# Performance work log

Measured on AMD Instinct MI355X. Metric: run time of the kernel, lower is better.

## Reference

```python
import jax, jax.numpy as jnp
import numpy as np

WIN = 8
NUM_HEADS = 4
DIM = 128


def _relative_position_index(ws):
    coords = np.stack(np.meshgrid(np.arange(ws), np.arange(ws), indexing='ij'))  # (2, ws, ws)
    cf = coords.reshape(2, -1)                      # (2, ws*ws)
    rel = (cf[:, :, None] - cf[:, None, :]).transpose(1, 2, 0).astype(np.int64)  # (N, N, 2)
    rel[..., 0] += ws - 1
    rel[..., 1] += ws - 1
    rel[..., 0] *= 2 * ws - 1
    return rel.sum(-1)                              # (N, N) int64


def setup_inputs() -> dict:
    key = jax.random.key(0)
    ks = jax.random.split(key, 8)
    B_, N, C = 4096, WIN * WIN, DIM
    nW = 4096
    x = jax.random.normal(ks[0], (B_, N, C), dtype=jnp.float32)
    mask = jax.random.normal(ks[1], (nW, N, N), dtype=jnp.float32)
    wq = jax.random.normal(ks[2], (C, C), dtype=jnp.float32) * 0.02
    bq = jnp.zeros((C,), dtype=jnp.float32)
    wkv = jax.random.normal(ks[3], (2 * C, C), dtype=jnp.float32) * 0.02
    bkv = jnp.zeros((2 * C,), dtype=jnp.float32)
    bias_table = jax.random.normal(ks[4], ((2 * WIN - 1) * (2 * WIN - 1), NUM_HEADS), dtype=jnp.float32) * 0.02
    wproj = jax.random.normal(ks[5], (C, C), dtype=jnp.float32) * 0.02
    bproj = jnp.zeros((C,), dtype=jnp.float32)
    rel_index = jnp.asarray(_relative_position_index(WIN))
    return {"x": x, "wq": wq, "bq": bq, "wkv": wkv, "bkv": bkv,
            "bias_table": bias_table, "wproj": wproj, "bproj": bproj,
            "mask": mask, "rel_index": rel_index}


def reference(x, wq, bq, wkv, bkv, bias_table, wproj, bproj, mask, rel_index):
    B_, N, C = x.shape
    H = NUM_HEADS
    d = C // H
    scale = d ** -0.5
    # qkv projection (attn_kv=None path)
    q = (x @ wq.T + bq).reshape(B_, N, H, d).transpose(0, 2, 1, 3)      # (B_, H, N, d)
    kv = (x @ wkv.T + bkv).reshape(B_, N, 2, H, d)
    k = kv[:, :, 0].transpose(0, 2, 1, 3)                               # (B_, H, N, d)
    v = kv[:, :, 1].transpose(0, 2, 1, 3)
    attn = jnp.einsum('bhnd,bhmd->bhnm', q * scale, k)                  # (B_, H, N, N)
    # relative position bias gather: (N*N,) -> (N, N, H) -> (H, N, N)
    rpb = bias_table[rel_index.reshape(-1)].reshape(N, N, H).transpose(2, 0, 1)
    attn = attn + rpb[None]
    # shifted-window mask: attn viewed as (B_//nW, nW, H, N, N) + mask (nW, 1, N, N)
    nW = mask.shape[0]
    attn = (attn.reshape(B_ // nW, nW, H, N, N) + mask[None, :, None]).reshape(B_, H, N, N)
    attn = jax.nn.softmax(attn, axis=-1)
    out = jnp.einsum('bhnm,bhmd->bhnd', attn, v).transpose(0, 2, 1, 3).reshape(B_, N, C)
    return out @ wproj.T + bproj
```

## Files before the change

kernel.cpp:

```cpp
#include <hip/hip_runtime.h>


typedef __bf16 bf16x8 __attribute__((ext_vector_type(8)));
typedef __bf16 bf16x4 __attribute__((ext_vector_type(4)));
typedef float f32x4 __attribute__((ext_vector_type(4)));

#define LOG2E 1.4426950408889634f
#define QSCALE (0.17677669529663687f * 1.4426950408889634f)

__global__ __launch_bounds__(256)
void prep_kernel(const float* __restrict__ wq,
                 const float* __restrict__ wkv,
                 const float* __restrict__ wp,
                 const float* __restrict__ bt,
                 const int* __restrict__ ri,
                 char* __restrict__ ws) {
  int t = blockIdx.x * 256 + (int)threadIdx.x;
  if (t < 8192) {
    int s = t >> 11;
    int c = t & 2047;
    int lane = c & 63, kk = (c >> 6) & 3, ct = c >> 8;
    int li = lane & 15, q4 = lane >> 4;
    int col = ct * 16 + li;
    int ko = kk * 32 + q4 * 8;
    const float* src = (s == 0) ? (wq + col * 128 + ko)
                     : (s == 1) ? (wkv + col * 128 + ko)
                     : (s == 2) ? (wkv + (col + 128) * 128 + ko)
                                : (wp + col * 128 + ko);
    bf16x8 v;
#pragma unroll
    for (int i = 0; i < 8; ++i) v[i] = (__bf16)src[i];
    *(bf16x8*)(ws + s * 32768 + c * 16) = v;
  } else {
    int c = t - 8192;
    int lane = c & 63, tj = (c >> 6) & 3, ti = (c >> 8) & 3, h = (c >> 10) & 3;
    int li = lane & 15, q4 = lane >> 4;
    int m = tj * 16 + li;
    f32x4 r;
#pragma unroll
    for (int rr = 0; rr < 4; ++rr) {
      int n = ti * 16 + q4 * 4 + rr;
      r[rr] = LOG2E * bt[ri[n * 64 + m] * 4 + h];
    }
    *(f32x4*)(ws + 131072 + c * 16) = r;
  }
}

static __device__ __forceinline__ bf16x8 cvt8(const float* __restrict__ p) {
  bf16x8 r;
#pragma unroll
  for (int i = 0; i < 8; ++i) r[i] = (__bf16)p[i];
  return r;
}

static __device__ __forceinline__ int xaddr(int r, int c) {
  return (r << 8) + ((((c >> 3) ^ (r & 7)) << 4)) + ((c & 7) << 1);
}
static __device__ __forceinline__ int qaddr(int r, int c) {
  return (r << 6) + ((((c >> 3) ^ ((r >> 2) & 3)) << 4)) + ((c & 7) << 1);
}
static __device__ __forceinline__ int paddr(int r, int c) {
  return (r << 7) + ((((c >> 3) ^ (r & 7)) << 4)) + ((c & 7) << 1);
}
static __device__ __forceinline__ int vtaddr(int dd, int m) {
  return (dd << 7) + ((((m >> 3) ^ (dd & 7)) << 4)) + ((m & 7) << 1);
}

#define MFMA16(acc, afr, bfr) \
  acc = __builtin_amdgcn_mfma_f32_16x16x32_bf16(afr, bfr, acc, 0, 0, 0)

__global__ __launch_bounds__(256, 3)
void winattn_kernel(const float* __restrict__ xg,
                    const float* __restrict__ bq,
                    const float* __restrict__ bkv,
                    const float* __restrict__ bp,
                    const float* __restrict__ mask,
                    const char* __restrict__ ws,
                    float* __restrict__ out) {
  __shared__ char smem[49152];
  const int b = blockIdx.x;
  const int tid = (int)threadIdx.x;
  const int h = tid >> 6;
  const int lane = tid & 63;
  const int q4 = lane >> 4;
  const int li = lane & 15;
  const int Wb = 16384 + h * 8192;
  const int Qb = Wb, Kb = Wb + 4096, Pb = Wb;
  const int Vb = h * 4096;
  const bf16x8* __restrict__ wqP = (const bf16x8*)(ws);
  const bf16x8* __restrict__ wkP = (const bf16x8*)(ws + 32768);
  const bf16x8* __restrict__ wvP = (const bf16x8*)(ws + 65536);
  const bf16x8* __restrict__ wpP = (const bf16x8*)(ws + 98304);
  const f32x4* __restrict__ rpbP = (const f32x4*)(ws + 131072);

  {
    const float* xw = xg + b * 8192;
#pragma unroll
    for (int rep = 0; rep < 4; ++rep) {
      int chunk = rep * 256 + tid;
      int r = chunk >> 4, cc = chunk & 15;
      bf16x8 v = cvt8(xw + r * 128 + cc * 8);
      *(bf16x8*)(smem + xaddr(r, cc * 8)) = v;
    }
  }
  __syncthreads();

  {
    f32x4 aqT[2][4] = {}; f32x4 akT[2][4] = {}; f32x4 av[4][2] = {};
#pragma unroll
    for (int kk = 0; kk < 4; ++kk) {
      bf16x8 a[4];
#pragma unroll
      for (int nt = 0; nt < 4; ++nt)
        a[nt] = *(const bf16x8*)(smem + xaddr(nt * 16 + li, kk * 32 + q4 * 8));
#pragma unroll
      for (int mt = 0; mt < 2; ++mt) {
        int wi = ((h * 2 + mt) * 4 + kk) * 64 + lane;
        bf16x8 wbq = wqP[wi];
        bf16x8 wbk = wkP[wi];
        bf16x8 wbv = wvP[wi];
#pragma unroll
        for (int nt = 0; nt < 4; ++nt) {
          MFMA16(aqT[mt][nt], wbq, a[nt]);
          MFMA16(akT[mt][nt], wbk, a[nt]);
          MFMA16(av[nt][mt], a[nt], wbv);
        }
      }
    }
#pragma unroll
    for (int mt = 0; mt < 2; ++mt) {
      f32x4 bq4 = *(const f32x4*)(bq + h * 32 + mt * 16 + q4 * 4);
      f32x4 bk4 = *(const f32x4*)(bkv + h * 32 + mt * 16 + q4 * 4);
      int f0 = mt * 16 + q4 * 4;
#pragma unroll
      for (int nt = 0; nt < 4; ++nt) {
        bf16x4 qv, kv;
#pragma unroll
        for (int rr = 0; rr < 4; ++rr) {
          qv[rr] = (__bf16)((aqT[mt][nt][rr] + bq4[rr]) * QSCALE);
          kv[rr] = (__bf16)(akT[mt][nt][rr] + bk4[rr]);
        }
        int row = nt * 16 + li;
        *(bf16x4*)(smem + Qb + qaddr(row, f0)) = qv;
        *(bf16x4*)(smem + Kb + qaddr(row, f0)) = kv;
      }
    }
    __syncthreads();
#pragma unroll
    for (int tj = 0; tj < 2; ++tj) {
      int col = h * 32 + tj * 16 + li;
      float bvv = bkv[col + 128];
      int lc = tj * 16 + li;
#pragma unroll
      for (int ti = 0; ti < 4; ++ti) {
        bf16x4 vv;
#pragma unroll
        for (int rr = 0; rr < 4; ++rr) vv[rr] = (__bf16)(av[ti][tj][rr] + bvv);
        *(bf16x4*)(smem + Vb + vtaddr(lc, ti * 16 + q4 * 4)) = vv;
      }
    }
  }
  asm volatile("s_waitcnt lgkmcnt(0)" ::: "memory");

  float bias[4][4][4];
  {
    const float* mw = mask + b * 4096;
#pragma unroll
    for (int ti = 0; ti < 4; ++ti)
#pragma unroll
      for (int tj = 0; tj < 4; ++tj) {
        f32x4 rv = rpbP[((h * 4 + ti) * 4 + tj) * 64 + lane];
        int m = tj * 16 + li;
#pragma unroll
        for (int rr = 0; rr < 4; ++rr) {
          int n = ti * 16 + q4 * 4 + rr;
          bias[ti][tj][rr] = fmaf(LOG2E, mw[n * 64 + m], rv[rr]);
        }
      }
  }

  f32x4 S[4][4];
  {
    bf16x8 qf[4], kf[4];
#pragma unroll
    for (int t = 0; t < 4; ++t) {
      qf[t] = *(const bf16x8*)(smem + Qb + qaddr(t * 16 + li, q4 * 8));
      kf[t] = *(const bf16x8*)(smem + Kb + qaddr(t * 16 + li, q4 * 8));
    }
#pragma unroll
    for (int ti = 0; ti < 4; ++ti)
#pragma unroll
      for (int tj = 0; tj < 4; ++tj) {
        f32x4 c = { bias[ti][tj][0], bias[ti][tj][1],
                    bias[ti][tj][2], bias[ti][tj][3] };
        S[ti][tj] = __builtin_amdgcn_mfma_f32_16x16x32_bf16(qf[ti], kf[tj], c, 0, 0, 0);
      }
  }

  float rinv[4][4];
#pragma unroll
  for (int ti = 0; ti < 4; ++ti)
#pragma unroll
    for (int rr = 0; rr < 4; ++rr) {
      float mx = fmaxf(fmaxf(S[ti][0][rr], S[ti][1][rr]),
                       fmaxf(S[ti][2][rr], S[ti][3][rr]));
      mx = fmaxf(mx, __shfl_xor(mx, 1));
      mx = fmaxf(mx, __shfl_xor(mx, 2));
      mx = fmaxf(mx, __shfl_xor(mx, 4));
      mx = fmaxf(mx, __shfl_xor(mx, 8));
      float s = 0.f;
#pragma unroll
      for (int tj = 0; tj < 4; ++tj) {
        float e = __builtin_amdgcn_exp2f(S[ti][tj][rr] - mx);
        S[ti][tj][rr] = e;
        s += e;
      }
      s += __shfl_xor(s, 1);
      s += __shfl_xor(s, 2);
      s += __shfl_xor(s, 4);
      s += __shfl_xor(s, 8);
      rinv[ti][rr] = __builtin_amdgcn_rcpf(s);
    }

#pragma unroll
  for (int ti = 0; ti < 4; ++ti)
#pragma unroll
    for (int rr = 0; rr < 4; ++rr) {
      int n = ti * 16 + q4 * 4 + rr;
#pragma unroll
      for (int tj = 0; tj < 4; ++tj) {
        int m = tj * 16 + li;
        *(__bf16*)(smem + Pb + paddr(n, m)) = (__bf16)S[ti][tj][rr];
      }
    }
  asm volatile("s_waitcnt lgkmcnt(0)" ::: "memory");

  f32x4 O[4][2] = {};
#pragma unroll
  for (int ks = 0; ks < 2; ++ks) {
    bf16x8 pf[4], vf[2];
#pragma unroll
    for (int ti = 0; ti < 4; ++ti)
      pf[ti] = *(const bf16x8*)(smem + Pb + paddr(ti * 16 + li, ks * 32 + q4 * 8));
#pragma unroll
    for (int tj = 0; tj < 2; ++tj)
      vf[tj] = *(const bf16x8*)(smem + Vb + vtaddr(tj * 16 + li, ks * 32 + q4 * 8));
#pragma unroll
    for (int ti = 0; ti < 4; ++ti)
#pragma unroll
      for (int tj = 0; tj < 2; ++tj)
        MFMA16(O[ti][tj], pf[ti], vf[tj]);
  }

  __syncthreads();
#pragma unroll
  for (int ti = 0; ti < 4; ++ti)
#pragma unroll
    for (int tj = 0; tj < 2; ++tj)
#pragma unroll
      for (int rr = 0; rr < 4; ++rr) {
        int row = ti * 16 + q4 * 4 + rr;
        int col = h * 32 + tj * 16 + li;
        *(__bf16*)(smem + xaddr(row, col)) = (__bf16)(O[ti][tj][rr] * rinv[ti][rr]);
      }
  __syncthreads();

  {
    f32x4 acc[4][2] = {};
#pragma unroll
    for (int kk = 0; kk < 4; ++kk) {
      bf16x8 a[4];
#pragma unroll
      for (int ti = 0; ti < 4; ++ti)
        a[ti] = *(const bf16x8*)(smem + xaddr(ti * 16 + li, kk * 32 + q4 * 8));
#pragma unroll
      for (int tj = 0; tj < 2; ++tj) {
        int wi = ((h * 2 + tj) * 4 + kk) * 64 + lane;
        bf16x8 wb = wpP[wi];
#pragma unroll
        for (int ti = 0; ti < 4; ++ti)
          MFMA16(acc[ti][tj], a[ti], wb);
      }
    }
    float* ow = out + b * 8192;
#pragma unroll
    for (int tj = 0; tj < 2; ++tj) {
      int col = h * 32 + tj * 16 + li;
      float bpv = bp[col];
#pragma unroll
      for (int ti = 0; ti < 4; ++ti)
#pragma unroll
        for (int rr = 0; rr < 4; ++rr) {
          int row = ti * 16 + q4 * 4 + rr;
          ow[row * 128 + col] = acc[ti][tj][rr] + bpv;
        }
    }
  }
}

extern "C" void kernel_launch(void* const* d_in, const int* in_sizes, int n_in,
                              void* d_out, int out_size, void* d_ws, size_t ws_size,
                              hipStream_t stream) {
  (void)in_sizes; (void)n_in; (void)ws_size; (void)out_size;
  prep_kernel<<<96, 256, 0, stream>>>(
      (const float*)d_in[1],
      (const float*)d_in[3],
      (const float*)d_in[6],
      (const float*)d_in[5],
      (const int*)d_in[9],
      (char*)d_ws);
  winattn_kernel<<<4096, 256, 0, stream>>>(
      (const float*)d_in[0],
      (const float*)d_in[2],
      (const float*)d_in[4],
      (const float*)d_in[7],
      (const float*)d_in[8],
      (const char*)d_ws,
      (float*)d_out);
}
```

Baseline: 347.2 us.

## Transpose score and projection MFMA layouts for vectorized mask loads and output stores

Computes the score tile as K·Qᵀ so each lane holds four consecutive key positions. Mask values can then be read as float4 nontemporal loads, and P can be written to shared memory as bf16x4 vectors. Softmax normalization moves before the PV product, so the reduction now uses two cross-lane shuffles over 16 values per lane. The output projection is likewise transposed so results go out as float4 nontemporal stores, and the x input is loaded with vector nontemporal loads. The main cost targeted is scalar global memory traffic for the mask and output; the risk is extra multiplies and a small rounding change from normalizing P before the bf16 cast.

```diff
diff --git a/kernel.cpp b/kernel.cpp
--- a/kernel.cpp
+++ b/kernel.cpp
@@ -35,21 +35,23 @@
     int c = t - 8192;
     int lane = c & 63, tj = (c >> 6) & 3, ti = (c >> 8) & 3, h = (c >> 10) & 3;
     int li = lane & 15, q4 = lane >> 4;
-    int m = tj * 16 + li;
+    int qt = tj * 16 + li;
     f32x4 r;
 #pragma unroll
     for (int rr = 0; rr < 4; ++rr) {
-      int n = ti * 16 + q4 * 4 + rr;
-      r[rr] = LOG2E * bt[ri[n * 64 + m] * 4 + h];
+      int kt = ti * 16 + q4 * 4 + rr;
+      r[rr] = LOG2E * bt[ri[qt * 64 + kt] * 4 + h];
     }
     *(f32x4*)(ws + 131072 + c * 16) = r;
   }
 }
 
-static __device__ __forceinline__ bf16x8 cvt8(const float* __restrict__ p) {
+static __device__ __forceinline__ bf16x8 cvt8nt(const float* __restrict__ p) {
+  f32x4 a = __builtin_nontemporal_load((const f32x4*)p);
+  f32x4 b = __builtin_nontemporal_load((const f32x4*)p + 1);
   bf16x8 r;
 #pragma unroll
-  for (int i = 0; i < 8; ++i) r[i] = (__bf16)p[i];
+  for (int i = 0; i < 4; ++i) { r[i] = (__bf16)a[i]; r[i + 4] = (__bf16)b[i]; }
   return r;
 }
 
@@ -99,7 +101,7 @@
     for (int rep = 0; rep < 4; ++rep) {
       int chunk = rep * 256 + tid;
       int r = chunk >> 4, cc = chunk & 15;
-      bf16x8 v = cvt8(xw + r * 128 + cc * 8);
+      bf16x8 v = cvt8nt(xw + r * 128 + cc * 8);
       *(bf16x8*)(smem + xaddr(r, cc * 8)) = v;
     }
   }
@@ -162,7 +164,7 @@
   }
   asm volatile("s_waitcnt lgkmcnt(0)" ::: "memory");
 
-  float bias[4][4][4];
+  f32x4 bias[4][4];
   {
     const float* mw = mask + b * 4096;
 #pragma unroll
@@ -170,12 +172,11 @@
 #pragma unroll
       for (int tj = 0; tj < 4; ++tj) {
         f32x4 rv = rpbP[((h * 4 + ti) * 4 + tj) * 64 + lane];
-        int m = tj * 16 + li;
-#pragma unroll
-        for (int rr = 0; rr < 4; ++rr) {
-          int n = ti * 16 + q4 * 4 + rr;
-          bias[ti][tj][rr] = fmaf(LOG2E, mw[n * 64 + m], rv[rr]);
-        }
+        f32x4 mv = __builtin_nontemporal_load(
+            (const f32x4*)(mw + (tj * 16 + li) * 64 + ti * 16 + q4 * 4));
+#pragma unroll
+        for (int rr = 0; rr < 4; ++rr) rv[rr] = fmaf(LOG2E, mv[rr], rv[rr]);
+        bias[ti][tj] = rv;
       }
   }
 
@@ -190,48 +191,46 @@
 #pragma unroll
     for (int ti = 0; ti < 4; ++ti)
 #pragma unroll
-      for (int tj = 0; tj < 4; ++tj) {
-        f32x4 c = { bias[ti][tj][0], bias[ti][tj][1],
-                    bias[ti][tj][2], bias[ti][tj][3] };
-        S[ti][tj] = __builtin_amdgcn_mfma_f32_16x16x32_bf16(qf[ti], kf[tj], c, 0, 0, 0);
-      }
-  }
-
-  float rinv[4][4];
-#pragma unroll
-  for (int ti = 0; ti < 4; ++ti)
-#pragma unroll
-    for (int rr = 0; rr < 4; ++rr) {
-      float mx = fmaxf(fmaxf(S[ti][0][rr], S[ti][1][rr]),
-                       fmaxf(S[ti][2][rr], S[ti][3][rr]));
-      mx = fmaxf(mx, __shfl_xor(mx, 1));
-      mx = fmaxf(mx, __shfl_xor(mx, 2));
-      mx = fmaxf(mx, __shfl_xor(mx, 4));
-      mx = fmaxf(mx, __shfl_xor(mx, 8));
-      float s = 0.f;
-#pragma unroll
-      for (int tj = 0; tj < 4; ++tj) {
+      for (int tj = 0; tj < 4; ++tj)
+        S[ti][tj] = __builtin_amdgcn_mfma_f32_16x16x32_bf16(
+            kf[ti], qf[tj], bias[ti][tj], 0, 0, 0);
+  }
+
+#pragma unroll
+  for (int tj = 0; tj < 4; ++tj) {
+    float mx = S[0][tj][0];
+#pragma unroll
+    for (int ti = 0; ti < 4; ++ti)
+#pragma unroll
+      for (int rr = 0; rr < 4; ++rr) mx = fmaxf(mx, S[ti][tj][rr]);
+    mx = fmaxf(mx, __shfl_xor(mx, 16));
+    mx = fmaxf(mx, __shfl_xor(mx, 32));
+    float s = 0.f;
+#pragma unroll
+    for (int ti = 0; ti < 4; ++ti)
+#pragma unroll
+      for (int rr = 0; rr < 4; ++rr) {
         float e = __builtin_amdgcn_exp2f(S[ti][tj][rr] - mx);
         S[ti][tj][rr] = e;
         s += e;
       }
-      s += __shfl_xor(s, 1);
-      s += __shfl_xor(s, 2);
-      s += __shfl_xor(s, 4);
-      s += __shfl_xor(s, 8);
-      rinv[ti][rr] = __builtin_amdgcn_rcpf(s);
-    }
+    s += __shfl_xor(s, 16);
+    s += __shfl_xor(s, 32);
+    float rinv = __builtin_amdgcn_rcpf(s);
+#pragma unroll
+    for (int ti = 0; ti < 4; ++ti)
+#pragma unroll
+      for (int rr = 0; rr < 4; ++rr) S[ti][tj][rr] *= rinv;
+  }
 
 #pragma unroll
   for (int ti = 0; ti < 4; ++ti)
 #pragma unroll
-    for (int rr = 0; rr < 4; ++rr) {
-      int n = ti * 16 + q4 * 4 + rr;
-#pragma unroll
-      for (int tj = 0; tj < 4; ++tj) {
-        int m = tj * 16 + li;
-        *(__bf16*)(smem + Pb + paddr(n, m)) = (__bf16)S[ti][tj][rr];
-      }
+    for (int tj = 0; tj < 4; ++tj) {
+      bf16x4 pv;
+#pragma unroll
+      for (int rr = 0; rr < 4; ++rr) pv[rr] = (__bf16)S[ti][tj][rr];
+      *(bf16x4*)(smem + Pb + paddr(tj * 16 + li, ti * 16 + q4 * 4)) = pv;
     }
   asm volatile("s_waitcnt lgkmcnt(0)" ::: "memory");
 
@@ -261,39 +260,39 @@
       for (int rr = 0; rr < 4; ++rr) {
         int row = ti * 16 + q4 * 4 + rr;
         int col = h * 32 + tj * 16 + li;
-        *(__bf16*)(smem + xaddr(row, col)) = (__bf16)(O[ti][tj][rr] * rinv[ti][rr]);
+        *(__bf16*)(smem + xaddr(row, col)) = (__bf16)O[ti][tj][rr];
       }
   __syncthreads();
 
   {
-    f32x4 acc[4][2] = {};
+    f32x4 acc[2][4] = {};
 #pragma unroll
     for (int kk = 0; kk < 4; ++kk) {
       bf16x8 a[4];
 #pragma unroll
-      for (int ti = 0; ti < 4; ++ti)
-        a[ti] = *(const bf16x8*)(smem + xaddr(ti * 16 + li, kk * 32 + q4 * 8));
-#pragma unroll
-      for (int tj = 0; tj < 2; ++tj) {
-        int wi = ((h * 2 + tj) * 4 + kk) * 64 + lane;
+      for (int nt = 0; nt < 4; ++nt)
+        a[nt] = *(const bf16x8*)(smem + xaddr(nt * 16 + li, kk * 32 + q4 * 8));
+#pragma unroll
+      for (int mt = 0; mt < 2; ++mt) {
+        int wi = ((h * 2 + mt) * 4 + kk) * 64 + lane;
         bf16x8 wb = wpP[wi];
 #pragma unroll
-        for (int ti = 0; ti < 4; ++ti)
-          MFMA16(acc[ti][tj], a[ti], wb);
+        for (int nt = 0; nt < 4; ++nt)
+          MFMA16(acc[mt][nt], wb, a[nt]);
       }
     }
     float* ow = out + b * 8192;
 #pragma unroll
-    for (int tj = 0; tj < 2; ++tj) {
-      int col = h * 32 + tj * 16 + li;
-      float bpv = bp[col];
-#pragma unroll
-      for (int ti = 0; ti < 4; ++ti)
-#pragma unroll
-        for (int rr = 0; rr < 4; ++rr) {
-          int row = ti * 16 + q4 * 4 + rr;
-          ow[row * 128 + col] = acc[ti][tj][rr] + bpv;
-        }
+    for (int mt = 0; mt < 2; ++mt) {
+      f32x4 bp4 = *(const f32x4*)(bp + h * 32 + mt * 16 + q4 * 4);
+#pragma unroll
+      for (int nt = 0; nt < 4; ++nt) {
+        f32x4 o;
+#pragma unroll
+        for (int rr = 0; rr < 4; ++rr) o[rr] = acc[mt][nt][rr] + bp4[rr];
+        __builtin_nontemporal_store(
+            o, (f32x4*)(ow + (nt * 16 + li) * 128 + h * 32 + mt * 16 + q4 * 4));
+      }
     }
   }
 }
```

Result: slower. 389.3 us (+12.1%).
